# Kernel tuning notes

Hardware: AMD Instinct MI355X
Metric: run time of the kernel (lower is better)

The kernel has to match this reference:

```python
import jax, jax.numpy as jnp
import numpy as np

N, C, T, H, W = 8, 512, 8, 32, 32
CI = 256          # inter_channels = in_channels // 2
CA = 128          # audio feature dim (hard-coded nn.Linear(128, in_channels))
BN_EPS = 1e-5
LN_EPS = 1e-5


def setup_inputs() -> dict:
    key = jax.random.key(0)
    ks = jax.random.split(key, 8)
    s = 0.02
    f32 = jnp.float32
    return {
        "x": jax.random.normal(ks[0], (N, C, T, H, W), f32),
        "audio": jax.random.normal(ks[1], (N, T, CA), f32),
        "align_W": jax.random.normal(ks[2], (C, CA), f32) * s,
        "align_b": jnp.zeros((C,), f32),
        "Wg": jax.random.normal(ks[3], (CI, C), f32) * s,
        "bg": jnp.zeros((CI,), f32),
        "Wth": jax.random.normal(ks[4], (CI, C), f32) * s,
        "bth": jnp.zeros((CI,), f32),
        "Wph": jax.random.normal(ks[5], (CI, C), f32) * s,
        "bph": jnp.zeros((CI,), f32),
        "Wz": jax.random.normal(ks[6], (C, CI), f32) * s,
        "bz": jnp.zeros((C,), f32),
        "bn_gamma": jnp.ones((C,), f32),
        "bn_beta": jnp.zeros((C,), f32),
        "ln_gamma": jnp.ones((C,), f32),
        "ln_beta": jnp.zeros((C,), f32),
    }


def reference(x, audio, align_W, align_b, Wg, bg, Wth, bth, Wph, bph,
              Wz, bz, bn_gamma, bn_beta, ln_gamma, ln_beta):
    n, c, t, h, w = x.shape
    thw = t * h * w

    # align_channel: Linear(128, C) + ReLU on audio (N,T,128) -> (N,T,C)
    audio_temp = jax.nn.relu(jnp.einsum('ntk,ck->ntc', audio, align_W) + align_b)
    a = audio_temp.transpose(0, 2, 1)  # (N,C,T); broadcast over (H,W) kept implicit

    # 1x1x1 conv projections (== per-token linear maps)
    g_x = (jnp.einsum('oc,ncthw->nthwo', Wg, x) + bg).reshape(n, thw, CI)      # (N,THW,CI)
    theta_x = (jnp.einsum('oc,ncthw->nthwo', Wth, x) + bth).reshape(n, thw, CI)
    phi_a = jnp.einsum('oc,nct->not', Wph, a) + bph[None, :, None]             # (N,CI,T)

    # mode='dot' attention. phi(audio) is constant over (h,w): the full score
    # matrix f[n,s,(t,h,w)] equals f_small[n,s,t], so f@g factorizes exactly.
    f_small = jnp.einsum('nsi,nit->nst', theta_x, phi_a)   # (N,THW,T)
    f_div = f_small / thw                                  # f / N_tokens
    G = g_x.reshape(n, t, h * w, CI).sum(axis=2)           # (N,T,CI): sum of g over repeated hw
    y = jnp.einsum('nst,nto->nso', f_div, G)               # (N,THW,CI)
    y = y.transpose(0, 2, 1).reshape(n, CI, t, h, w)

    # W_z: 1x1x1 conv (CI->C) + BatchNorm3d (training-mode batch stats)
    W_y = jnp.einsum('oc,ncthw->nothw', Wz, y) + bz[None, :, None, None, None]
    mu = W_y.mean(axis=(0, 2, 3, 4), keepdims=True)
    var = W_y.var(axis=(0, 2, 3, 4), keepdims=True)
    W_y = (W_y - mu) * jax.lax.rsqrt(var + BN_EPS)
    W_y = W_y * bn_gamma[None, :, None, None, None] + bn_beta[None, :, None, None, None]

    # residual blend + LayerNorm over channel dim
    z = 0.5 * W_y + 0.5 * x
    zp = z.transpose(0, 2, 3, 4, 1)  # (N,T,H,W,C)
    mu2 = zp.mean(axis=-1, keepdims=True)
    var2 = zp.var(axis=-1, keepdims=True)
    zp = (zp - mu2) * jax.lax.rsqrt(var2 + LN_EPS) * ln_gamma + ln_beta
    z = zp.transpose(0, 4, 1, 2, 3)  # (N,C,T,H,W)
    return z, audio_temp
```

## Files before the change

### kernel.cpp

```cpp
#include <hip/hip_runtime.h>


typedef float __attribute__((ext_vector_type(2))) f32x2;

__device__ __forceinline__ float hsum4(float4 v) { return (v.x + v.y) + (v.z + v.w); }
__device__ __forceinline__ void fma4v(float4& a, float4 w, float4 x) {
    a.x = fmaf(w.x, x.x, a.x); a.y = fmaf(w.y, x.y, a.y);
    a.z = fmaf(w.z, x.z, a.z); a.w = fmaf(w.w, x.w, a.w);
}

__global__ __launch_bounds__(256) void k_stage1(
    const float* __restrict__ x, const float* __restrict__ audio,
    const float* __restrict__ alignW, const float* __restrict__ alignB,
    const float* __restrict__ Wph, const float* __restrict__ bph,
    const float* __restrict__ Wth, const float* __restrict__ bth,
    float* __restrict__ outA, float* __restrict__ constT, float* __restrict__ M,
    float* __restrict__ xsT)
{
    int b = blockIdx.x; int tid = threadIdx.x;
    __shared__ float al[128];
    __shared__ float atl[512];
    __shared__ float phil[256];
    __shared__ float red[256];
    if (b >= 64) {
        int row = (b - 64) * 4 + (tid >> 6);
        int lane = tid & 63;
        const float4* p = reinterpret_cast<const float4*>(x + (size_t)row * 1024);
        float s = 0.f;
        #pragma unroll
        for (int k = 0; k < 4; ++k) {
            float4 v = p[lane + 64 * k];
            s += v.x + v.y + v.z + v.w;
        }
        for (int off = 32; off > 0; off >>= 1) s += __shfl_down(s, off);
        if (lane == 0) {
            int n = row >> 12, c = (row >> 3) & 511, t = row & 7;
            xsT[((size_t)n * 8 + t) * 512 + c] = s;
        }
        return;
    }
    int n = b >> 3; int t = b & 7;
    if (tid < 32)
        reinterpret_cast<float4*>(al)[tid] =
            reinterpret_cast<const float4*>(audio + (n * 8 + t) * 128)[tid];
    __syncthreads();
    {
        const float4* W0 = reinterpret_cast<const float4*>(alignW + (size_t)tid * 128);
        const float4* W1 = reinterpret_cast<const float4*>(alignW + (size_t)(tid + 256) * 128);
        const float4* A4 = reinterpret_cast<const float4*>(al);
        float4 s00 = {0,0,0,0}, s01 = {0,0,0,0}, s10 = {0,0,0,0}, s11 = {0,0,0,0};
        #pragma unroll
        for (int k = 0; k < 32; k += 2) {
            float4 a0 = A4[k], a1 = A4[k + 1];
            fma4v(s00, W0[k], a0); fma4v(s01, W0[k + 1], a1);
            fma4v(s10, W1[k], a0); fma4v(s11, W1[k + 1], a1);
        }
        float v0 = fmaxf(alignB[tid] + hsum4(s00) + hsum4(s01), 0.f);
        float v1 = fmaxf(alignB[tid + 256] + hsum4(s10) + hsum4(s11), 0.f);
        atl[tid] = v0;       outA[(n * 8 + t) * 512 + tid] = v0;
        atl[tid + 256] = v1; outA[(n * 8 + t) * 512 + tid + 256] = v1;
    }
    __syncthreads();
    {
        const float4* Wp = reinterpret_cast<const float4*>(Wph + (size_t)tid * 512);
        const float4* At = reinterpret_cast<const float4*>(atl);
        float4 s0 = {0,0,0,0}, s1 = {0,0,0,0}, s2 = {0,0,0,0}, s3 = {0,0,0,0};
        #pragma unroll 4
        for (int k = 0; k < 128; k += 4) {
            fma4v(s0, Wp[k], At[k]);         fma4v(s1, Wp[k + 1], At[k + 1]);
            fma4v(s2, Wp[k + 2], At[k + 2]); fma4v(s3, Wp[k + 3], At[k + 3]);
        }
        float acc = bph[tid] + (hsum4(s0) + hsum4(s1)) + (hsum4(s2) + hsum4(s3));
        phil[tid] = acc;
        red[tid] = acc * bth[tid];
    }
    __syncthreads();
    for (int sr = 128; sr > 0; sr >>= 1) {
        if (tid < sr) red[tid] += red[tid + sr];
        __syncthreads();
    }
    if (tid == 0) constT[n * 8 + t] = red[0];
    {
        float a0 = 0, a1 = 0, a2 = 0, a3 = 0, c0 = 0, c1 = 0, c2 = 0, c3 = 0;
        #pragma unroll 2
        for (int i = 0; i < 256; i += 4) {
            float p0 = phil[i], p1 = phil[i + 1], p2 = phil[i + 2], p3 = phil[i + 3];
            const float* W = Wth + (size_t)i * 512 + tid;
            a0 = fmaf(W[0], p0, a0);    a1 = fmaf(W[512], p1, a1);
            a2 = fmaf(W[1024], p2, a2); a3 = fmaf(W[1536], p3, a3);
            const float* W2 = W + 256;
            c0 = fmaf(W2[0], p0, c0);    c1 = fmaf(W2[512], p1, c1);
            c2 = fmaf(W2[1024], p2, c2); c3 = fmaf(W2[1536], p3, c3);
        }
        M[n * 4096 + tid * 8 + t] = (a0 + a1) + (a2 + a3);
        M[n * 4096 + (tid + 256) * 8 + t] = (c0 + c1) + (c2 + c3);
    }
}

__global__ __launch_bounds__(512, 4) void k_stage2(
    const float* __restrict__ x, const float* __restrict__ M,
    const float* __restrict__ constT, const float* __restrict__ xsT,
    const float* __restrict__ Wg, const float* __restrict__ bg,
    const float* __restrict__ Wz,
    float* __restrict__ fs, float* __restrict__ Part, float* __restrict__ GW)
{
    int b = blockIdx.x; int tid = threadIdx.x;
    __shared__ float Ml[512][8];
    __shared__ float ldsT[8][8][130];
    __shared__ float partm[2][44];
    __shared__ float xsl[512];
    __shared__ float gl[256];
    if (b >= 512) {
        int b2 = b - 512; int n = b2 >> 3; int t = b2 & 7;
        xsl[tid] = xsT[((size_t)n * 8 + t) * 512 + tid];
        __syncthreads();
        if (tid < 256) {
            const float4* Wr = reinterpret_cast<const float4*>(Wg + (size_t)tid * 512);
            const float4* X4 = reinterpret_cast<const float4*>(xsl);
            float4 s0 = {0,0,0,0}, s1 = {0,0,0,0}, s2 = {0,0,0,0}, s3 = {0,0,0,0};
            #pragma unroll 4
            for (int k = 0; k < 128; k += 4) {
                fma4v(s0, Wr[k], X4[k]);         fma4v(s1, Wr[k + 1], X4[k + 1]);
                fma4v(s2, Wr[k + 2], X4[k + 2]); fma4v(s3, Wr[k + 3], X4[k + 3]);
            }
            gl[tid] = 1024.f * bg[tid] + (hsum4(s0) + hsum4(s1)) + (hsum4(s2) + hsum4(s3));
        }
        __syncthreads();
        {
            const float4* Wr = reinterpret_cast<const float4*>(Wz + (size_t)tid * 256);
            const float4* G4 = reinterpret_cast<const float4*>(gl);
            float4 s0 = {0,0,0,0}, s1 = {0,0,0,0}, s2 = {0,0,0,0}, s3 = {0,0,0,0};
            #pragma unroll 4
            for (int k = 0; k < 64; k += 4) {
                fma4v(s0, Wr[k], G4[k]);         fma4v(s1, Wr[k + 1], G4[k + 1]);
                fma4v(s2, Wr[k + 2], G4[k + 2]); fma4v(s3, Wr[k + 3], G4[k + 3]);
            }
            GW[((size_t)n * 8 + t) * 512 + tid] =
                (hsum4(s0) + hsum4(s1)) + (hsum4(s2) + hsum4(s3));
        }
        return;
    }
    int n = b >> 6; int s0i = (b & 63) << 7;
    int lane = tid & 63; int wv = tid >> 6;
    {
        const float4* src = reinterpret_cast<const float4*>(M + n * 4096);
        float4* dst = reinterpret_cast<float4*>(&Ml[0][0]);
        for (int i = tid; i < 1024; i += 512) dst[i] = src[i];
    }
    __syncthreads();
    const float* xb = x + (size_t)n * 4194304 + s0i + lane * 2;
    float2 p2[8];
    #pragma unroll
    for (int k = 0; k < 8; ++k) p2[k] = make_float2(0.f, 0.f);
    #pragma unroll 16
    for (int j = 0; j < 64; ++j) {
        int c = wv * 64 + j;
        float2 xv = *reinterpret_cast<const float2*>(xb + (size_t)c * 8192);
        float4 m0 = *reinterpret_cast<const float4*>(&Ml[c][0]);
        float4 m1 = *reinterpret_cast<const float4*>(&Ml[c][4]);
        p2[0].x = fmaf(xv.x, m0.x, p2[0].x); p2[0].y = fmaf(xv.y, m0.x, p2[0].y);
        p2[1].x = fmaf(xv.x, m0.y, p2[1].x); p2[1].y = fmaf(xv.y, m0.y, p2[1].y);
        p2[2].x = fmaf(xv.x, m0.z, p2[2].x); p2[2].y = fmaf(xv.y, m0.z, p2[2].y);
        p2[3].x = fmaf(xv.x, m0.w, p2[3].x); p2[3].y = fmaf(xv.y, m0.w, p2[3].y);
        p2[4].x = fmaf(xv.x, m1.x, p2[4].x); p2[4].y = fmaf(xv.y, m1.x, p2[4].y);
        p2[5].x = fmaf(xv.x, m1.y, p2[5].x); p2[5].y = fmaf(xv.y, m1.y, p2[5].y);
        p2[6].x = fmaf(xv.x, m1.z, p2[6].x); p2[6].y = fmaf(xv.y, m1.z, p2[6].y);
        p2[7].x = fmaf(xv.x, m1.w, p2[7].x); p2[7].y = fmaf(xv.y, m1.w, p2[7].y);
    }
    #pragma unroll
    for (int k = 0; k < 8; ++k)
        *reinterpret_cast<float2*>(&ldsT[wv][k][lane * 2]) = p2[k];
    __syncthreads();
    if (tid < 128) {
        int tok = tid; int wq = tid >> 6;
        const float* ct = constT + n * 8;
        float q[8];
        #pragma unroll
        for (int k = 0; k < 8; ++k) {
            float v = ct[k];
            #pragma unroll
            for (int g = 0; g < 8; ++g) v += ldsT[g][k][tok];
            q[k] = v;
        }
        float4* op = reinterpret_cast<float4*>(fs + ((size_t)n * 8192 + s0i + tok) * 8);
        op[0] = make_float4(q[0], q[1], q[2], q[3]);
        op[1] = make_float4(q[4], q[5], q[6], q[7]);
        float mom[44];
        {
            int idx = 8;
            for (int t1 = 0; t1 < 8; ++t1) {
                mom[t1] = q[t1];
                for (int t2 = t1; t2 < 8; ++t2) { mom[idx] = q[t1] * q[t2]; ++idx; }
            }
        }
        for (int k = 0; k < 44; ++k)
            for (int off = 32; off > 0; off >>= 1) mom[k] += __shfl_down(mom[k], off);
        if ((tid & 63) == 0)
            for (int k = 0; k < 44; ++k) partm[wq][k] = mom[k];
    }
    __syncthreads();
    if (tid < 44) Part[b * 44 + tid] = partm[0][tid] + partm[1][tid];
}

__global__ __launch_bounds__(512) void k_bn(
    const float* __restrict__ Part, const float* __restrict__ GW,
    const float* __restrict__ bz, const float* __restrict__ bng, const float* __restrict__ bnb,
    const float* __restrict__ lng, const float* __restrict__ lnb,
    float* __restrict__ pack0, float* __restrict__ gw2)
{
    int n0 = blockIdx.x; int c = threadIdx.x;
    __shared__ float Fl[64];
    __shared__ float S2l[512];
    if (c < 352) {
        int n = c / 44, k = c % 44;
        float v = 0.f;
        for (int i = 0; i < 64; ++i) v += Part[(n * 64 + i) * 44 + k];
        if (k < 8) Fl[n * 8 + k] = v;
        else {
            int kk = k - 8; int t1 = 0;
            while (kk >= 8 - t1) { kk -= 8 - t1; ++t1; }
            int t2 = t1 + kk;
            S2l[n * 64 + t1 * 8 + t2] = v;
            S2l[n * 64 + t2 * 8 + t1] = v;
        }
    }
    __syncthreads();
    const float r = 1.f / 8192.f;
    float meanu = 0.f, e2 = 0.f;
    float gmine[8];
    for (int n2 = 0; n2 < 8; ++n2) {
        float g[8];
        #pragma unroll
        for (int t = 0; t < 8; ++t) g[t] = GW[(n2 * 8 + t) * 512 + c];
        if (n2 == n0) {
            #pragma unroll
            for (int t = 0; t < 8; ++t) gmine[t] = g[t];
        }
        #pragma unroll
        for (int t = 0; t < 8; ++t) meanu += Fl[n2 * 8 + t] * g[t];
        for (int t1 = 0; t1 < 8; ++t1)
            #pragma unroll
            for (int t2 = 0; t2 < 8; ++t2) e2 += S2l[n2 * 64 + t1 * 8 + t2] * g[t1] * g[t2];
    }
    const float invCnt = 1.f / 65536.f;
    meanu *= r * invCnt;
    e2 *= r * r * invCnt;
    float var = fmaxf(e2 - meanu * meanu, 0.f);
    float bzv = bz[c];
    float sc = bng[c] * rsqrtf(var + 1e-5f);
    float sh = bnb[c] - (meanu + bzv) * sc;
    if (n0 == 0) {
        float4 pk;
        pk.x = 0.5f * (bzv * sc + sh);
        pk.y = lng[c];
        pk.z = lnb[c];
        pk.w = 0.f;
        *reinterpret_cast<float4*>(pack0 + c * 4) = pk;
    }
    float scale = 0.5f * r * sc;
    #pragma unroll
    for (int t = 0; t < 8; ++t)
        gw2[((size_t)n0 * 512 + c) * 8 + t] = gmine[t] * scale;
}

__global__ __launch_bounds__(512, 4) void k_final(
    const float* __restrict__ x, const float* __restrict__ fs,
    const float* __restrict__ pack0, const float* __restrict__ gw2,
    float* __restrict__ outZ)
{
    int b = blockIdx.x; int n = b >> 6; int s0 = (b & 63) << 7;
    int tid = threadIdx.x; int lane = tid & 63; int wv = tid >> 6;
    __shared__ float GWl[512][8];
    __shared__ float4 PKl[512];
    __shared__ float redS[2][8][130];
    {
        const float4* src = reinterpret_cast<const float4*>(gw2 + (size_t)n * 4096);
        float4* dst = reinterpret_cast<float4*>(&GWl[0][0]);
        for (int i = tid; i < 1024; i += 512) dst[i] = src[i];
        PKl[tid] = reinterpret_cast<const float4*>(pack0)[tid];
    }
    __syncthreads();
    float4 fA0, fB0, fA1, fB1;
    {
        const float4* fp = reinterpret_cast<const float4*>(fs + ((size_t)n * 8192 + s0 + lane * 2) * 8);
        fA0 = fp[0]; fB0 = fp[1]; fA1 = fp[2]; fB1 = fp[3];
    }
    const size_t xbase = (size_t)n * 4194304 + s0 + lane * 2;
    float2 s1 = make_float2(0.f, 0.f), sq = make_float2(0.f, 0.f);
    #pragma unroll 16
    for (int j = 0; j < 64; ++j) {
        int c = wv * 64 + j;
        float2 xv = *reinterpret_cast<const float2*>(&x[xbase + (size_t)c * 8192]);
        float4 g0 = *reinterpret_cast<const float4*>(&GWl[c][0]);
        float4 g1 = *reinterpret_cast<const float4*>(&GWl[c][4]);
        float pk0 = PKl[c].x;
        float z0 = pk0 + 0.5f * xv.x
            + fA0.x * g0.x + fA0.y * g0.y + fA0.z * g0.z + fA0.w * g0.w
            + fB0.x * g1.x + fB0.y * g1.y + fB0.z * g1.z + fB0.w * g1.w;
        float z1 = pk0 + 0.5f * xv.y
            + fA1.x * g0.x + fA1.y * g0.y + fA1.z * g0.z + fA1.w * g0.w
            + fB1.x * g1.x + fB1.y * g1.y + fB1.z * g1.z + fB1.w * g1.w;
        s1.x += z0; sq.x += z0 * z0;
        s1.y += z1; sq.y += z1 * z1;
    }
    *reinterpret_cast<float2*>(&redS[0][wv][lane * 2]) = s1;
    *reinterpret_cast<float2*>(&redS[1][wv][lane * 2]) = sq;
    __syncthreads();
    float mean0, rstd0, mean1, rstd1;
    {
        int t0 = lane * 2, t1 = lane * 2 + 1;
        float a0 = 0.f, q0 = 0.f, a1 = 0.f, q1 = 0.f;
        #pragma unroll
        for (int g = 0; g < 8; ++g) {
            a0 += redS[0][g][t0]; q0 += redS[1][g][t0];
            a1 += redS[0][g][t1]; q1 += redS[1][g][t1];
        }
        mean0 = a0 * (1.f / 512.f);
        rstd0 = rsqrtf(fmaxf(q0 * (1.f / 512.f) - mean0 * mean0, 0.f) + 1e-5f);
        mean1 = a1 * (1.f / 512.f);
        rstd1 = rsqrtf(fmaxf(q1 * (1.f / 512.f) - mean1 * mean1, 0.f) + 1e-5f);
    }
    #pragma unroll 16
    for (int j = 0; j < 64; ++j) {
        int c = wv * 64 + j;
        float2 xv = *reinterpret_cast<const float2*>(&x[xbase + (size_t)c * 8192]);
        float4 g0 = *reinterpret_cast<const float4*>(&GWl[c][0]);
        float4 g1 = *reinterpret_cast<const float4*>(&GWl[c][4]);
        float4 pk = PKl[c];
        float z0 = pk.x + 0.5f * xv.x
            + fA0.x * g0.x + fA0.y * g0.y + fA0.z * g0.z + fA0.w * g0.w
            + fB0.x * g1.x + fB0.y * g1.y + fB0.z * g1.z + fB0.w * g1.w;
        float z1 = pk.x + 0.5f * xv.y
            + fA1.x * g0.x + fA1.y * g0.y + fA1.z * g0.z + fA1.w * g0.w
            + fB1.x * g1.x + fB1.y * g1.y + fB1.z * g1.z + fB1.w * g1.w;
        f32x2 o;
        o.x = (z0 - mean0) * rstd0 * pk.y + pk.z;
        o.y = (z1 - mean1) * rstd1 * pk.y + pk.z;
        __builtin_nontemporal_store(o, reinterpret_cast<f32x2*>(&outZ[xbase + (size_t)c * 8192]));
    }
}

extern "C" void kernel_launch(void* const* d_in, const int* in_sizes, int n_in,
                              void* d_out, int out_size, void* d_ws, size_t ws_size,
                              hipStream_t stream)
{
    const float* x      = (const float*)d_in[0];
    const float* audio  = (const float*)d_in[1];
    const float* alignW = (const float*)d_in[2];
    const float* alignB = (const float*)d_in[3];
    const float* Wg     = (const float*)d_in[4];
    const float* bg     = (const float*)d_in[5];
    const float* Wth    = (const float*)d_in[6];
    const float* bth    = (const float*)d_in[7];
    const float* Wph    = (const float*)d_in[8];
    const float* bph    = (const float*)d_in[9];
    const float* Wz     = (const float*)d_in[10];
    const float* bz     = (const float*)d_in[11];
    const float* bng    = (const float*)d_in[12];
    const float* bnb    = (const float*)d_in[13];
    const float* lng    = (const float*)d_in[14];
    const float* lnb    = (const float*)d_in[15];
    float* outZ = (float*)d_out;
    float* outA = outZ + 33554432;

    uintptr_t pa = ((uintptr_t)d_ws + 255) & ~(uintptr_t)255;
    float* w = (float*)pa;

    float* constT = w;
    float* M      = w + 64;
    float* XS     = w + 32832;
    float* GW     = w + 65600;
    float* Part   = w + 98368;
    float* pack0  = w + 120896;
    float* gw2    = w + 122944;
    float* fsm    = w + 155712;

    k_stage1<<<8256, 256, 0, stream>>>(x, audio, alignW, alignB, Wph, bph, Wth, bth,
                                       outA, constT, M, XS);
    k_stage2<<<576, 512, 0, stream>>>(x, M, constT, XS, Wg, bg, Wz, fsm, Part, GW);
    k_bn<<<8, 512, 0, stream>>>(Part, GW, bz, bng, bnb, lng, lnb, pack0, gw2);
    k_final<<<512, 512, 0, stream>>>(x, fsm, pack0, gw2, outZ);
}
```

Before: 172.0 us.

## Move x row-sum reduction into stage-2 kernel and split G/GW into separate launch

The per-(n,c,t) spatial sum of x moves from the first kernel into the second, where it runs alongside the attention-score blocks. The G and W_z·G matvecs become a new small kernel launched afterwards. The first kernel now handles only the 64 audio blocks, so the x-sum pass overlaps the score computation instead of running before it. The cost is one extra kernel launch and a narrow 64-block tail kernel.

```diff
diff --git a/kernel.cpp b/kernel.cpp
--- a/kernel.cpp
+++ b/kernel.cpp
@@ -9,37 +9,19 @@
     a.z = fmaf(w.z, x.z, a.z); a.w = fmaf(w.w, x.w, a.w);
 }
 
-__global__ __launch_bounds__(256) void k_stage1(
-    const float* __restrict__ x, const float* __restrict__ audio,
+__global__ __launch_bounds__(256) void k_A(
+    const float* __restrict__ audio,
     const float* __restrict__ alignW, const float* __restrict__ alignB,
     const float* __restrict__ Wph, const float* __restrict__ bph,
     const float* __restrict__ Wth, const float* __restrict__ bth,
-    float* __restrict__ outA, float* __restrict__ constT, float* __restrict__ M,
-    float* __restrict__ xsT)
+    float* __restrict__ outA, float* __restrict__ constT, float* __restrict__ M)
 {
     int b = blockIdx.x; int tid = threadIdx.x;
+    int n = b >> 3; int t = b & 7;
     __shared__ float al[128];
     __shared__ float atl[512];
     __shared__ float phil[256];
     __shared__ float red[256];
-    if (b >= 64) {
-        int row = (b - 64) * 4 + (tid >> 6);
-        int lane = tid & 63;
-        const float4* p = reinterpret_cast<const float4*>(x + (size_t)row * 1024);
-        float s = 0.f;
-        #pragma unroll
-        for (int k = 0; k < 4; ++k) {
-            float4 v = p[lane + 64 * k];
-            s += v.x + v.y + v.z + v.w;
-        }
-        for (int off = 32; off > 0; off >>= 1) s += __shfl_down(s, off);
-        if (lane == 0) {
-            int n = row >> 12, c = (row >> 3) & 511, t = row & 7;
-            xsT[((size_t)n * 8 + t) * 512 + c] = s;
-        }
-        return;
-    }
-    int n = b >> 3; int t = b & 7;
     if (tid < 32)
         reinterpret_cast<float4*>(al)[tid] =
             reinterpret_cast<const float4*>(audio + (n * 8 + t) * 128)[tid];
@@ -97,51 +79,33 @@
     }
 }
 
-__global__ __launch_bounds__(512, 4) void k_stage2(
+__global__ __launch_bounds__(512, 4) void k_B(
     const float* __restrict__ x, const float* __restrict__ M,
-    const float* __restrict__ constT, const float* __restrict__ xsT,
-    const float* __restrict__ Wg, const float* __restrict__ bg,
-    const float* __restrict__ Wz,
-    float* __restrict__ fs, float* __restrict__ Part, float* __restrict__ GW)
+    const float* __restrict__ constT, float* __restrict__ fs,
+    float* __restrict__ Part, float* __restrict__ xsT)
 {
     int b = blockIdx.x; int tid = threadIdx.x;
+    int lane = tid & 63; int wv = tid >> 6;
     __shared__ float Ml[512][8];
     __shared__ float ldsT[8][8][130];
     __shared__ float partm[2][44];
-    __shared__ float xsl[512];
-    __shared__ float gl[256];
     if (b >= 512) {
-        int b2 = b - 512; int n = b2 >> 3; int t = b2 & 7;
-        xsl[tid] = xsT[((size_t)n * 8 + t) * 512 + tid];
-        __syncthreads();
-        if (tid < 256) {
-            const float4* Wr = reinterpret_cast<const float4*>(Wg + (size_t)tid * 512);
-            const float4* X4 = reinterpret_cast<const float4*>(xsl);
-            float4 s0 = {0,0,0,0}, s1 = {0,0,0,0}, s2 = {0,0,0,0}, s3 = {0,0,0,0};
-            #pragma unroll 4
-            for (int k = 0; k < 128; k += 4) {
-                fma4v(s0, Wr[k], X4[k]);         fma4v(s1, Wr[k + 1], X4[k + 1]);
-                fma4v(s2, Wr[k + 2], X4[k + 2]); fma4v(s3, Wr[k + 3], X4[k + 3]);
-            }
-            gl[tid] = 1024.f * bg[tid] + (hsum4(s0) + hsum4(s1)) + (hsum4(s2) + hsum4(s3));
-        }
-        __syncthreads();
-        {
-            const float4* Wr = reinterpret_cast<const float4*>(Wz + (size_t)tid * 256);
-            const float4* G4 = reinterpret_cast<const float4*>(gl);
-            float4 s0 = {0,0,0,0}, s1 = {0,0,0,0}, s2 = {0,0,0,0}, s3 = {0,0,0,0};
-            #pragma unroll 4
-            for (int k = 0; k < 64; k += 4) {
-                fma4v(s0, Wr[k], G4[k]);         fma4v(s1, Wr[k + 1], G4[k + 1]);
-                fma4v(s2, Wr[k + 2], G4[k + 2]); fma4v(s3, Wr[k + 3], G4[k + 3]);
-            }
-            GW[((size_t)n * 8 + t) * 512 + tid] =
-                (hsum4(s0) + hsum4(s1)) + (hsum4(s2) + hsum4(s3));
+        int row = (b - 512) * 8 + wv;
+        const float4* p = reinterpret_cast<const float4*>(x + (size_t)row * 1024);
+        float s = 0.f;
+        #pragma unroll
+        for (int k = 0; k < 4; ++k) {
+            float4 v = p[lane + 64 * k];
+            s += v.x + v.y + v.z + v.w;
+        }
+        for (int off = 32; off > 0; off >>= 1) s += __shfl_down(s, off);
+        if (lane == 0) {
+            int n = row >> 12, c = (row >> 3) & 511, t = row & 7;
+            xsT[((size_t)n * 8 + t) * 512 + c] = s;
         }
         return;
     }
     int n = b >> 6; int s0i = (b & 63) << 7;
-    int lane = tid & 63; int wv = tid >> 6;
     {
         const float4* src = reinterpret_cast<const float4*>(M + n * 4096);
         float4* dst = reinterpret_cast<float4*>(&Ml[0][0]);
@@ -202,6 +166,42 @@
     if (tid < 44) Part[b * 44 + tid] = partm[0][tid] + partm[1][tid];
 }
 
+__global__ __launch_bounds__(512) void k_GGW(
+    const float* __restrict__ xsT, const float* __restrict__ Wg,
+    const float* __restrict__ bg, const float* __restrict__ Wz,
+    float* __restrict__ GW)
+{
+    int b2 = blockIdx.x; int n = b2 >> 3; int t = b2 & 7; int tid = threadIdx.x;
+    __shared__ float xsl[512];
+    __shared__ float gl[256];
+    xsl[tid] = xsT[((size_t)n * 8 + t) * 512 + tid];
+    __syncthreads();
+    if (tid < 256) {
+        const float4* Wr = reinterpret_cast<const float4*>(Wg + (size_t)tid * 512);
+        const float4* X4 = reinterpret_cast<const float4*>(xsl);
+        float4 s0 = {0,0,0,0}, s1 = {0,0,0,0}, s2 = {0,0,0,0}, s3 = {0,0,0,0};
+        #pragma unroll 4
+        for (int k = 0; k < 128; k += 4) {
+            fma4v(s0, Wr[k], X4[k]);         fma4v(s1, Wr[k + 1], X4[k + 1]);
+            fma4v(s2, Wr[k + 2], X4[k + 2]); fma4v(s3, Wr[k + 3], X4[k + 3]);
+        }
+        gl[tid] = 1024.f * bg[tid] + (hsum4(s0) + hsum4(s1)) + (hsum4(s2) + hsum4(s3));
+    }
+    __syncthreads();
+    {
+        const float4* Wr = reinterpret_cast<const float4*>(Wz + (size_t)tid * 256);
+        const float4* G4 = reinterpret_cast<const float4*>(gl);
+        float4 s0 = {0,0,0,0}, s1 = {0,0,0,0}, s2 = {0,0,0,0}, s3 = {0,0,0,0};
+        #pragma unroll 4
+        for (int k = 0; k < 64; k += 4) {
+            fma4v(s0, Wr[k], G4[k]);         fma4v(s1, Wr[k + 1], G4[k + 1]);
+            fma4v(s2, Wr[k + 2], G4[k + 2]); fma4v(s3, Wr[k + 3], G4[k + 3]);
+        }
+        GW[((size_t)n * 8 + t) * 512 + tid] =
+            (hsum4(s0) + hsum4(s1)) + (hsum4(s2) + hsum4(s3));
+    }
+}
+
 __global__ __launch_bounds__(512) void k_bn(
     const float* __restrict__ Part, const float* __restrict__ GW,
     const float* __restrict__ bz, const float* __restrict__ bng, const float* __restrict__ bnb,
@@ -375,9 +375,10 @@
     float* gw2    = w + 122944;
     float* fsm    = w + 155712;
 
-    k_stage1<<<8256, 256, 0, stream>>>(x, audio, alignW, alignB, Wph, bph, Wth, bth,
-                                       outA, constT, M, XS);
-    k_stage2<<<576, 512, 0, stream>>>(x, M, constT, XS, Wg, bg, Wz, fsm, Part, GW);
+    k_A<<<64, 256, 0, stream>>>(audio, alignW, alignB, Wph, bph, Wth, bth,
+                                outA, constT, M);
+    k_B<<<4608, 512, 0, stream>>>(x, M, constT, fsm, Part, XS);
+    k_GGW<<<64, 512, 0, stream>>>(XS, Wg, bg, Wz, GW);
     k_bn<<<8, 512, 0, stream>>>(Part, GW, bz, bng, bnb, lng, lnb, pack0, gw2);
     k_final<<<512, 512, 0, stream>>>(x, fsm, pack0, gw2, outZ);
 }
```

New measurement: 180.0 us. +4.6%, slower.
